# Kernel tuning notes

Hardware: AMD Instinct MI355X
Metric: run time of the kernel (lower is better)

The kernel has to match this reference:

```python
import jax, jax.numpy as jnp
import numpy as np

SEARCH = (4, 6, 8)

def _round_ste(v):
    return v + jax.lax.stop_gradient(jnp.round(v) - v)

def _fake_quant(x, alpha, k_bits):
    # PAMS quant_act: clamp to [-alpha, alpha], uniform fake-quant with STE round
    a = jnp.abs(alpha)
    s = (2.0 ** (k_bits - 1) - 1.0) / a
    return _round_ste(jnp.clip(x, -a, a) * s) / s

def setup_inputs() -> dict:
    key = jax.random.key(0)
    k0, k1 = jax.random.split(key, 2)
    B, C, H, W = 16, 64, 256, 256
    x = jax.random.normal(k0, (B, C, H, W), jnp.float32)
    grad_feat = jax.random.normal(k1, (B, 2), jnp.float32)
    bits = jnp.zeros((B,), jnp.float32)
    weighted_bits = jnp.zeros((B,), jnp.float32)
    Wl = jnp.ones((3, C + 2), jnp.float32)              # nn.init.ones_
    bl = jnp.array([0.0, 0.0, 1.0], jnp.float32)        # zeros_, bias[-1]=1
    alpha1 = jnp.full((1,), 10.0, jnp.float32)          # PAMS alpha init
    alpha2 = jnp.full((1,), 10.0, jnp.float32)
    alpha3 = jnp.full((1,), 10.0, jnp.float32)
    return dict(x=x, grad_feat=grad_feat, bits=bits, weighted_bits=weighted_bits,
                Wl=Wl, bl=bl, alpha1=alpha1, alpha2=alpha2, alpha3=alpha3)

def reference(x, grad_feat, bits, weighted_bits, Wl, bl, alpha1, alpha2, alpha3):
    sg = jax.lax.stop_gradient
    # std over spatial dims, unbiased (torch default), detached -> [B, C]
    layer_std = sg(jnp.std(x, axis=(2, 3), ddof=1))
    x_embed = jnp.concatenate([grad_feat, layer_std], axis=1)   # [B, C+2]
    bit_type = x_embed @ Wl.T + bl                              # [B, 3]
    flag = jnp.argmax(bit_type, axis=1)                         # [B]
    p = jax.nn.softmax(bit_type, axis=1)
    p1, p2, p3 = p[:, 0], p[:, 1], p[:, 2]
    bits_hard = ((flag == 0) * SEARCH[0] + (flag == 1) * SEARCH[1]
                 + (flag == 2) * SEARCH[2]).astype(x.dtype)
    bits_soft = p1 * SEARCH[0] + p2 * SEARCH[1] + p3 * SEARCH[2]
    bits_out = sg(bits_hard) - sg(bits_soft) + bits_soft        # STE on bit count
    bits = bits + bits_out
    denom = sg(SEARCH[0] * p1 + SEARCH[1] * p2 + SEARCH[2] * p3)
    weighted_bits = weighted_bits + bits_out / denom
    q1 = _fake_quant(x, alpha1[0], SEARCH[0])
    q2 = _fake_quant(x, alpha2[0], SEARCH[1])
    q3 = _fake_quant(x, alpha3[0], SEARCH[2])
    w1 = p1[:, None, None, None]; w2 = p2[:, None, None, None]; w3 = p3[:, None, None, None]
    out_soft = w1 * q1 + w2 * q2 + w3 * q3
    m1 = (flag == 0)[:, None, None, None].astype(x.dtype)
    m2 = (flag == 1)[:, None, None, None].astype(x.dtype)
    m3 = (flag == 2)[:, None, None, None].astype(x.dtype)
    out_hard = m1 * q1 + m2 * q2 + m3 * q3
    residual = sg(out_hard) - sg(out_soft) + out_soft           # STE hard/soft gate
    return grad_feat, residual, bits, weighted_bits
```

## Files before the change

kernel.cpp:

```cpp
#include <hip/hip_runtime.h>
#include <math.h>

typedef float fx4 __attribute__((ext_vector_type(4)));

__global__ void bitsel_std_kernel(const float4* __restrict__ x,
                                  float* __restrict__ std_out,
                                  int n4 ) {
    const size_t base = (size_t)blockIdx.x * (size_t)n4;
    float sum = 0.f, sq = 0.f;
    for (int i = threadIdx.x; i < n4; i += blockDim.x) {
        float4 v = x[base + i];
        sum += (v.x + v.y) + (v.z + v.w);
        sq  += v.x * v.x + v.y * v.y + v.z * v.z + v.w * v.w;
    }
    for (int off = 32; off > 0; off >>= 1) {
        sum += __shfl_down(sum, off);
        sq  += __shfl_down(sq,  off);
    }
    __shared__ float s_sum[8], s_sq[8];
    const int wave = threadIdx.x >> 6;
    if ((threadIdx.x & 63) == 0) { s_sum[wave] = sum; s_sq[wave] = sq; }
    __syncthreads();
    if (threadIdx.x == 0) {
        float S = 0.f, Q = 0.f;
        const int nw = blockDim.x >> 6;
        for (int w = 0; w < nw; ++w) { S += s_sum[w]; Q += s_sq[w]; }
        const float N = (float)(n4 * 4);
        float var = (Q - S * S / N) / (N - 1.f);
        std_out[blockIdx.x] = sqrtf(fmaxf(var, 0.f));
    }
}

__global__ void bitsel_head_kernel(const float* __restrict__ gf,
                                   const float* __restrict__ bits_in,
                                   const float* __restrict__ wbits_in,
                                   const float* __restrict__ Wl,
                                   const float* __restrict__ bl,
                                   const float* __restrict__ a1,
                                   const float* __restrict__ a2,
                                   const float* __restrict__ a3,
                                   const float* __restrict__ stds,
                                   float* __restrict__ out,
                                   float* __restrict__ ws_a,
                                   float* __restrict__ ws_s,
                                   int B, int C, size_t Ntot ) {
    const int t = threadIdx.x;
    if (t < 2 * B) out[t] = gf[t];
    if (t < B) {
        const int b = t;
        const int D = C + 2;
        float bt[3];
        for (int k = 0; k < 3; ++k) {
            float acc = gf[2 * b] * Wl[k * D] + gf[2 * b + 1] * Wl[k * D + 1];
            for (int c = 0; c < C; ++c) acc += stds[b * C + c] * Wl[k * D + 2 + c];
            bt[k] = acc + bl[k];
        }
        int flag = 0; float m = bt[0];
        if (bt[1] > m) { m = bt[1]; flag = 1; }
        if (bt[2] > m) { m = bt[2]; flag = 2; }
        float e0 = expf(bt[0] - m), e1 = expf(bt[1] - m), e2 = expf(bt[2] - m);
        float esum = e0 + e1 + e2;
        float p1 = e0 / esum, p2 = e1 / esum, p3 = e2 / esum;
        float bits_hard = (flag == 0) ? 4.f : (flag == 1) ? 6.f : 8.f;
        float bits_soft = 4.f * p1 + 6.f * p2 + 8.f * p3;
        float bits_out  = (bits_hard - bits_soft) + bits_soft;
        float denom     = 4.f * p1 + 6.f * p2 + 8.f * p3;
        out[2 * B + Ntot + b]     = bits_in[b] + bits_out;
        out[2 * B + Ntot + B + b] = wbits_in[b] + bits_out / denom;
        float alpha = (flag == 0) ? a1[0] : (flag == 1) ? a2[0] : a3[0];
        float a = fabsf(alpha);
        float s = (exp2f(bits_hard - 1.f) - 1.f) / a;
        ws_a[b] = a;
        ws_s[b] = s;
    }
}

__global__ void bitsel_quant_kernel(const fx4* __restrict__ x,
                                    const float* __restrict__ ws_a,
                                    const float* __restrict__ ws_s,
                                    fx4* __restrict__ res,
                                    int per_b4 ,
                                    int chunk4 ,
                                    int nchunks) {
    const int g = nchunks - 1 - (int)blockIdx.x;
    const size_t start = (size_t)g * (size_t)chunk4;
    const int b = (int)(start / (size_t)per_b4);
    const float a = ws_a[b];
    const float s = ws_s[b];
    for (int i = threadIdx.x; i < chunk4; i += blockDim.x) {
        fx4 v = x[start + i];
        fx4 r;
        r.x = rintf(fminf(fmaxf(v.x, -a), a) * s) / s;
        r.y = rintf(fminf(fmaxf(v.y, -a), a) * s) / s;
        r.z = rintf(fminf(fmaxf(v.z, -a), a) * s) / s;
        r.w = rintf(fminf(fmaxf(v.w, -a), a) * s) / s;
        __builtin_nontemporal_store(r, &res[start + i]);
    }
}

extern "C" void kernel_launch(void* const* d_in, const int* in_sizes, int n_in,
                              void* d_out, int out_size, void* d_ws, size_t ws_size,
                              hipStream_t stream) {
    const float* x     = (const float*)d_in[0];
    const float* gf    = (const float*)d_in[1];
    const float* bits  = (const float*)d_in[2];
    const float* wbits = (const float*)d_in[3];
    const float* Wl    = (const float*)d_in[4];
    const float* bl    = (const float*)d_in[5];
    const float* a1    = (const float*)d_in[6];
    const float* a2    = (const float*)d_in[7];
    const float* a3    = (const float*)d_in[8];
    float* out = (float*)d_out;

    const int B   = in_sizes[2];
    const int C   = in_sizes[4] / 3 - 2;
    const int HWn = in_sizes[0] / (B * C);
    const int BC  = B * C;
    const int n4  = HWn / 4;
    const int per_b4 = (C * HWn) / 4;
    const size_t Ntot = (size_t)in_sizes[0];
    const int total4 = in_sizes[0] / 4;
    const int chunk4 = 4096;
    const int nchunks = total4 / chunk4;

    float* ws_std = (float*)d_ws;
    float* ws_a   = ws_std + BC;
    float* ws_s   = ws_a + B;

    bitsel_std_kernel<<<BC, 256, 0, stream>>>((const float4*)x, ws_std, n4);

    bitsel_head_kernel<<<1, 64, 0, stream>>>(gf, bits, wbits, Wl, bl, a1, a2, a3,
                                             ws_std, out, ws_a, ws_s, B, C, Ntot);

    bitsel_quant_kernel<<<nchunks, 256, 0, stream>>>((const fx4*)x, ws_a, ws_s,
                                                     (fx4*)(out + 2 * B),
                                                     per_b4, chunk4, nchunks);
}
```

Baseline: 144.5 us.

## Pipeline std reduction and quantization across batch groups in one fused kernel

Replaces the separate std, head and quant kernels with a single kernel launched once per group of four batch items. Each launch runs the quantization of the previous group while computing partial std sums for the current group. The head MLP is recomputed inside every quant block from the partial sums, which removes the serial head launch. The intent is to keep the second read of x close in time to the first so it can hit in the large cache, and to overlap the two phases. The cost is redundant head computation in every block and extra kernel launches.

```diff
diff --git a/kernel.cpp b/kernel.cpp
--- a/kernel.cpp
+++ b/kernel.cpp
@@ -2,99 +2,117 @@
 #include <math.h>
 
 typedef float fx4 __attribute__((ext_vector_type(4)));
+#define TPB 256
 
-__global__ void bitsel_std_kernel(const float4* __restrict__ x,
-                                  float* __restrict__ std_out,
-                                  int n4 ) {
-    const size_t base = (size_t)blockIdx.x * (size_t)n4;
-    float sum = 0.f, sq = 0.f;
-    for (int i = threadIdx.x; i < n4; i += blockDim.x) {
-        float4 v = x[base + i];
-        sum += (v.x + v.y) + (v.z + v.w);
-        sq  += v.x * v.x + v.y * v.y + v.z * v.z + v.w * v.w;
-    }
-    for (int off = 32; off > 0; off >>= 1) {
-        sum += __shfl_down(sum, off);
-        sq  += __shfl_down(sq,  off);
-    }
-    __shared__ float s_sum[8], s_sq[8];
-    const int wave = threadIdx.x >> 6;
-    if ((threadIdx.x & 63) == 0) { s_sum[wave] = sum; s_sq[wave] = sq; }
-    __syncthreads();
-    if (threadIdx.x == 0) {
-        float S = 0.f, Q = 0.f;
-        const int nw = blockDim.x >> 6;
-        for (int w = 0; w < nw; ++w) { S += s_sum[w]; Q += s_sq[w]; }
-        const float N = (float)(n4 * 4);
-        float var = (Q - S * S / N) / (N - 1.f);
-        std_out[blockIdx.x] = sqrtf(fmaxf(var, 0.f));
-    }
-}
+__global__ __launch_bounds__(TPB)
+void bitsel_rq_kernel(const fx4* __restrict__ x,
+                      const float* __restrict__ gf,
+                      const float* __restrict__ bits_in,
+                      const float* __restrict__ wbits_in,
+                      const float* __restrict__ Wl,
+                      const float* __restrict__ bl,
+                      const float* __restrict__ a1,
+                      const float* __restrict__ a2,
+                      const float* __restrict__ a3,
+                      float* __restrict__ out,
+                      fx4* __restrict__ res,
+                      float* __restrict__ part,
+                      int gR, int gQ, int nQ,
+                      int B, int C, int GB, int n4, int ppc,
+                      size_t Ntot) {
+    const int tid = threadIdx.x;
 
-__global__ void bitsel_head_kernel(const float* __restrict__ gf,
-                                   const float* __restrict__ bits_in,
-                                   const float* __restrict__ wbits_in,
-                                   const float* __restrict__ Wl,
-                                   const float* __restrict__ bl,
-                                   const float* __restrict__ a1,
-                                   const float* __restrict__ a2,
-                                   const float* __restrict__ a3,
-                                   const float* __restrict__ stds,
-                                   float* __restrict__ out,
-                                   float* __restrict__ ws_a,
-                                   float* __restrict__ ws_s,
-                                   int B, int C, size_t Ntot ) {
-    const int t = threadIdx.x;
-    if (t < 2 * B) out[t] = gf[t];
-    if (t < B) {
-        const int b = t;
-        const int D = C + 2;
-        float bt[3];
-        for (int k = 0; k < 3; ++k) {
-            float acc = gf[2 * b] * Wl[k * D] + gf[2 * b + 1] * Wl[k * D + 1];
-            for (int c = 0; c < C; ++c) acc += stds[b * C + c] * Wl[k * D + 2 + c];
-            bt[k] = acc + bl[k];
+    if ((int)blockIdx.x >= nQ) {
+        const int j  = (int)blockIdx.x - nQ;
+        const int ch = j / ppc;
+        const int pp = j % ppc;
+        const int q4 = n4 / ppc;
+        const size_t base = (size_t)(gR * GB * C + ch) * (size_t)n4 + (size_t)pp * q4;
+        float sum = 0.f, sq = 0.f;
+        for (int i = tid; i < q4; i += TPB) {
+            fx4 v = x[base + i];
+            sum += (v.x + v.y) + (v.z + v.w);
+            sq  += v.x * v.x + v.y * v.y + v.z * v.z + v.w * v.w;
         }
-        int flag = 0; float m = bt[0];
-        if (bt[1] > m) { m = bt[1]; flag = 1; }
-        if (bt[2] > m) { m = bt[2]; flag = 2; }
-        float e0 = expf(bt[0] - m), e1 = expf(bt[1] - m), e2 = expf(bt[2] - m);
-        float esum = e0 + e1 + e2;
-        float p1 = e0 / esum, p2 = e1 / esum, p3 = e2 / esum;
-        float bits_hard = (flag == 0) ? 4.f : (flag == 1) ? 6.f : 8.f;
-        float bits_soft = 4.f * p1 + 6.f * p2 + 8.f * p3;
-        float bits_out  = (bits_hard - bits_soft) + bits_soft;
-        float denom     = 4.f * p1 + 6.f * p2 + 8.f * p3;
-        out[2 * B + Ntot + b]     = bits_in[b] + bits_out;
-        out[2 * B + Ntot + B + b] = wbits_in[b] + bits_out / denom;
-        float alpha = (flag == 0) ? a1[0] : (flag == 1) ? a2[0] : a3[0];
-        float a = fabsf(alpha);
-        float s = (exp2f(bits_hard - 1.f) - 1.f) / a;
-        ws_a[b] = a;
-        ws_s[b] = s;
-    }
-}
+        for (int off = 32; off > 0; off >>= 1) {
+            sum += __shfl_down(sum, off);
+            sq  += __shfl_down(sq,  off);
+        }
+        __shared__ float ssum[4], ssq[4];
+        const int wv = tid >> 6;
+        if ((tid & 63) == 0) { ssum[wv] = sum; ssq[wv] = sq; }
+        __syncthreads();
+        if (tid == 0) {
+            float S = ssum[0] + ssum[1] + ssum[2] + ssum[3];
+            float Q = ssq[0]  + ssq[1]  + ssq[2]  + ssq[3];
+            const size_t idx = ((size_t)gR * (GB * C) + ch) * ppc + pp;
+            part[idx * 2 + 0] = S;
+            part[idx * 2 + 1] = Q;
+        }
+    } else {
+        const int k = (int)blockIdx.x;
+        const int qblk4 = (GB * C * n4) / nQ;
+        const int bpb   = nQ / GB;
+        const int bl_   = k / bpb;
+        const int b     = gQ * GB + bl_;
 
-__global__ void bitsel_quant_kernel(const fx4* __restrict__ x,
-                                    const float* __restrict__ ws_a,
-                                    const float* __restrict__ ws_s,
-                                    fx4* __restrict__ res,
-                                    int per_b4 ,
-                                    int chunk4 ,
-                                    int nchunks) {
-    const int g = nchunks - 1 - (int)blockIdx.x;
-    const size_t start = (size_t)g * (size_t)chunk4;
-    const int b = (int)(start / (size_t)per_b4);
-    const float a = ws_a[b];
-    const float s = ws_s[b];
-    for (int i = threadIdx.x; i < chunk4; i += blockDim.x) {
-        fx4 v = x[start + i];
-        fx4 r;
-        r.x = rintf(fminf(fmaxf(v.x, -a), a) * s) / s;
-        r.y = rintf(fminf(fmaxf(v.y, -a), a) * s) / s;
-        r.z = rintf(fminf(fmaxf(v.z, -a), a) * s) / s;
-        r.w = rintf(fminf(fmaxf(v.w, -a), a) * s) / s;
-        __builtin_nontemporal_store(r, &res[start + i]);
+        __shared__ float s_std[128];
+        __shared__ float s_as[2];
+
+        if (tid < C) {
+            const size_t idx = ((size_t)gQ * (GB * C) + (size_t)bl_ * C + tid) * ppc;
+            float S = 0.f, Qq = 0.f;
+            for (int p = 0; p < ppc; ++p) {
+                S  += part[(idx + p) * 2 + 0];
+                Qq += part[(idx + p) * 2 + 1];
+            }
+            const float N = (float)n4 * 4.f;
+            float var = (Qq - S * S / N) / (N - 1.f);
+            s_std[tid] = sqrtf(fmaxf(var, 0.f));
+        }
+        __syncthreads();
+        if (tid == 0) {
+            const int D = C + 2;
+            float bt[3];
+            for (int kk = 0; kk < 3; ++kk) {
+                float acc = gf[2 * b] * Wl[kk * D] + gf[2 * b + 1] * Wl[kk * D + 1];
+                for (int cc = 0; cc < C; ++cc) acc += s_std[cc] * Wl[kk * D + 2 + cc];
+                bt[kk] = acc + bl[kk];
+            }
+            int flag = 0; float m = bt[0];
+            if (bt[1] > m) { m = bt[1]; flag = 1; }
+            if (bt[2] > m) { m = bt[2]; flag = 2; }
+            float e0 = expf(bt[0] - m), e1 = expf(bt[1] - m), e2 = expf(bt[2] - m);
+            float esum = e0 + e1 + e2;
+            float p1 = e0 / esum, p2 = e1 / esum, p3 = e2 / esum;
+            float bits_hard = (flag == 0) ? 4.f : (flag == 1) ? 6.f : 8.f;
+            float bits_soft = 4.f * p1 + 6.f * p2 + 8.f * p3;
+            float bits_out  = (bits_hard - bits_soft) + bits_soft;
+            float denom     = 4.f * p1 + 6.f * p2 + 8.f * p3;
+            float alpha = (flag == 0) ? a1[0] : (flag == 1) ? a2[0] : a3[0];
+            float a  = fabsf(alpha);
+            float sc = (exp2f(bits_hard - 1.f) - 1.f) / a;
+            s_as[0] = a; s_as[1] = sc;
+            if (k % bpb == 0) {
+                out[2 * b]     = gf[2 * b];
+                out[2 * b + 1] = gf[2 * b + 1];
+                out[2 * B + Ntot + b]     = bits_in[b] + bits_out;
+                out[2 * B + Ntot + B + b] = wbits_in[b] + bits_out / denom;
+            }
+        }
+        __syncthreads();
+        const float a  = s_as[0];
+        const float sc = s_as[1];
+        const size_t start = (size_t)(gQ * GB * C) * (size_t)n4 + (size_t)k * qblk4;
+        for (int i = tid; i < qblk4; i += TPB) {
+            fx4 v = x[start + i];
+            fx4 r;
+            r.x = rintf(fminf(fmaxf(v.x, -a), a) * sc) / sc;
+            r.y = rintf(fminf(fmaxf(v.y, -a), a) * sc) / sc;
+            r.z = rintf(fminf(fmaxf(v.z, -a), a) * sc) / sc;
+            r.w = rintf(fminf(fmaxf(v.w, -a), a) * sc) / sc;
+            __builtin_nontemporal_store(r, &res[start + i]);
+        }
     }
 }
 
@@ -115,24 +133,26 @@
     const int B   = in_sizes[2];
     const int C   = in_sizes[4] / 3 - 2;
     const int HWn = in_sizes[0] / (B * C);
-    const int BC  = B * C;
     const int n4  = HWn / 4;
-    const int per_b4 = (C * HWn) / 4;
+    const int GB  = 4;
+    const int NG  = B / GB;
+    const int ppc = 4;
+    const int nR  = GB * C * ppc;
+    const int nQ  = GB * C * n4 / 4096;
     const size_t Ntot = (size_t)in_sizes[0];
-    const int total4 = in_sizes[0] / 4;
-    const int chunk4 = 4096;
-    const int nchunks = total4 / chunk4;
 
-    float* ws_std = (float*)d_ws;
-    float* ws_a   = ws_std + BC;
-    float* ws_s   = ws_a + B;
+    float* part = (float*)d_ws;
+    fx4* res = (fx4*)(out + 2 * B);
 
-    bitsel_std_kernel<<<BC, 256, 0, stream>>>((const float4*)x, ws_std, n4);
-
-    bitsel_head_kernel<<<1, 64, 0, stream>>>(gf, bits, wbits, Wl, bl, a1, a2, a3,
-                                             ws_std, out, ws_a, ws_s, B, C, Ntot);
-
-    bitsel_quant_kernel<<<nchunks, 256, 0, stream>>>((const fx4*)x, ws_a, ws_s,
-                                                     (fx4*)(out + 2 * B),
-                                                     per_b4, chunk4, nchunks);
+    bitsel_rq_kernel<<<nR, TPB, 0, stream>>>(
+        (const fx4*)x, gf, bits, wbits, Wl, bl, a1, a2, a3,
+        out, res, part, 0, -1, 0, B, C, GB, n4, ppc, Ntot);
+    for (int g = 1; g < NG; ++g) {
+        bitsel_rq_kernel<<<nQ + nR, TPB, 0, stream>>>(
+            (const fx4*)x, gf, bits, wbits, Wl, bl, a1, a2, a3,
+            out, res, part, g, g - 1, nQ, B, C, GB, n4, ppc, Ntot);
+    }
+    bitsel_rq_kernel<<<nQ, TPB, 0, stream>>>(
+        (const fx4*)x, gf, bits, wbits, Wl, bl, a1, a2, a3,
+        out, res, part, -1, NG - 1, nQ, B, C, GB, n4, ppc, Ntot);
 }
```

Measured after the change: 136.8 us. 1.06x faster.
